# Kernel tuning notes

Measured on AMD Instinct MI355X. Metric: run time of the kernel, lower is better.

## Reference

```python
import jax, jax.numpy as jnp
import numpy as np

K, D = 16384, 128

def setup_inputs() -> dict:
    key = jax.random.key(0)
    k1, k2 = jax.random.split(key)
    parts = jax.random.normal(k1, (K, D), dtype=jnp.float32)
    centers = jax.random.normal(k2, (K, D), dtype=jnp.float32)
    return {"parts": parts, "centers": centers}

def reference(parts, centers):
    # logits[e, j] = parts[e] . centers[j]  -> [K, K]
    logits = jnp.einsum('ed,kd->ek', parts, centers)
    # loss = -mean_e log_softmax(logits[e])[e]  (stable equivalent of
    # log(exp(logits[e,e]) / sum_j exp(logits[e,j])))
    logp = jax.nn.log_softmax(logits, axis=-1)
    diag = jnp.diagonal(logp)  # [K]
    return -jnp.mean(diag)
```

## Files before the change

### kernel.cpp

```cpp
#include <hip/hip_runtime.h>
#include <hip/hip_bf16.h>


#define K_DIM 16384
#define D_DIM 128
#define NSPLIT 32
#define COLS_PER_SPLIT (K_DIM / NSPLIT)
#define TILES_PER_SPLIT (COLS_PER_SPLIT / 32)
#define NROUND (TILES_PER_SPLIT / 2)

typedef __attribute__((ext_vector_type(8)))  int    i32x8;
typedef __attribute__((ext_vector_type(16))) float  f32x16;
typedef __attribute__((ext_vector_type(4)))  float  f32x4;
typedef __attribute__((ext_vector_type(2)))  float  f32x2;

__device__ __forceinline__ unsigned pack_fp8x4(float f0, float f1, float f2, float f3) {
    int r = 0;
    r = __builtin_amdgcn_cvt_pk_fp8_f32(f0, f1, r, false);
    r = __builtin_amdgcn_cvt_pk_fp8_f32(f2, f3, r, true);
    return (unsigned)r;
}

__global__ void convert_kernel(const float* __restrict__ parts,
                               const float* __restrict__ centers,
                               unsigned* __restrict__ pb8,
                               unsigned* __restrict__ cb8,
                               float* __restrict__ rowdot) {
    const float LOG2E = 1.4426950408889634f;
    int i = blockIdx.x * blockDim.x + threadIdx.x;
    const int lane = threadIdx.x & 63;

    f32x4 p = reinterpret_cast<const f32x4*>(parts)[i];
    f32x4 c = reinterpret_cast<const f32x4*>(centers)[i];
    pb8[i] = pack_fp8x4(p[0] * LOG2E, p[1] * LOG2E, p[2] * LOG2E, p[3] * LOG2E);
    cb8[i] = pack_fp8x4(c[0], c[1], c[2], c[3]);

    const int j = (i * 4) >> 7;
    float dd = p[0] * c[0] + p[1] * c[1] + p[2] * c[2] + p[3] * c[3];
#pragma unroll
    for (int off = 16; off > 0; off >>= 1)
        dd += __shfl_xor(dd, off);
    if ((lane & 31) == 0)
        rowdot[j] = dd;
}

__launch_bounds__(256, 4)
__global__ void lse_gemm_kernel(const unsigned char* __restrict__ P8,
                                const unsigned char* __restrict__ C8,
                                float* __restrict__ Sout) {
    __shared__ __attribute__((aligned(128))) unsigned char As[2][2][4096];

    const int bid   = blockIdx.x;
    const int xcd    = bid & 7;
    const int k      = bid >> 3;
    const int split  = xcd * 4 + (k & 3);
    const int rowblk = k >> 2;
    const int tid   = threadIdx.x;
    const int lane  = tid & 63;
    const int w     = tid >> 6;
    const int l31   = lane & 31;
    const int hi    = lane >> 5;
    const int rowgrp = rowblk * 4 + w;
    const int e0    = rowgrp * 64;
    const int e_lo  = e0 + l31;
    const int e_hi  = e0 + 32 + l31;

    i32x8 bl0, bl1, bh0, bh1;
    {
        const unsigned char* plo = P8 + (size_t)e_lo * D_DIM + hi * 32;
        const unsigned char* phi = P8 + (size_t)e_hi * D_DIM + hi * 32;
#pragma unroll
        for (int q = 0; q < 4; ++q) {
            bl0[q]     = reinterpret_cast<const int*>(plo)[q];
            bl1[q]     = reinterpret_cast<const int*>(plo + 64)[q];
            bh0[q]     = reinterpret_cast<const int*>(phi)[q];
            bh1[q]     = reinterpret_cast<const int*>(phi + 64)[q];
            bl0[q + 4] = reinterpret_cast<const int*>(plo + 16)[q];
            bl1[q + 4] = reinterpret_cast<const int*>(plo + 80)[q];
            bh0[q + 4] = reinterpret_cast<const int*>(phi + 16)[q];
            bh1[q + 4] = reinterpret_cast<const int*>(phi + 80)[q];
        }
    }

    const int j0 = split * COLS_PER_SPLIT;
    const int j_w = tid >> 3;
    const int d_w = (tid & 7) * 16;
    const unsigned char* gsrc = C8 + (size_t)(j0 + j_w) * D_DIM + d_w;
    const int woff = j_w * 128 + (d_w ^ ((j_w & 7) << 4));

    const int swz = (l31 & 7) << 4;
    const int rbase = l31 * 128;
    const int rk0a = rbase + (((hi * 32))      ^ swz);
    const int rk0b = rbase + (((hi * 32) + 16) ^ swz);
    const int rk1a = rbase + (((64 + hi * 32))      ^ swz);
    const int rk1b = rbase + (((64 + hi * 32) + 16) ^ swz);

    const f32x16 zc = {};
    float s0 = 0.f, s1 = 0.f;

    auto expsum = [&](const f32x16& acc) -> float {
        f32x2 v0 = {__builtin_amdgcn_exp2f(acc[0]),  __builtin_amdgcn_exp2f(acc[1])};
        f32x2 v1 = {__builtin_amdgcn_exp2f(acc[2]),  __builtin_amdgcn_exp2f(acc[3])};
        f32x2 v2 = {__builtin_amdgcn_exp2f(acc[4]),  __builtin_amdgcn_exp2f(acc[5])};
        f32x2 v3 = {__builtin_amdgcn_exp2f(acc[6]),  __builtin_amdgcn_exp2f(acc[7])};
        f32x2 v4 = {__builtin_amdgcn_exp2f(acc[8]),  __builtin_amdgcn_exp2f(acc[9])};
        f32x2 v5 = {__builtin_amdgcn_exp2f(acc[10]), __builtin_amdgcn_exp2f(acc[11])};
        f32x2 v6 = {__builtin_amdgcn_exp2f(acc[12]), __builtin_amdgcn_exp2f(acc[13])};
        f32x2 v7 = {__builtin_amdgcn_exp2f(acc[14]), __builtin_amdgcn_exp2f(acc[15])};
        v0 += v1; v2 += v3; v4 += v5; v6 += v7;
        v0 += v2; v4 += v6;
        v0 += v4;
        return v0[0] + v0[1];
    };

    auto mfma_tile = [&](const unsigned char* base, f32x16& acc0, f32x16& acc1) {
        i32x8 a0, a1;
#pragma unroll
        for (int q = 0; q < 4; ++q) {
            a0[q]     = reinterpret_cast<const int*>(base + rk0a)[q];
            a0[q + 4] = reinterpret_cast<const int*>(base + rk0b)[q];
            a1[q]     = reinterpret_cast<const int*>(base + rk1a)[q];
            a1[q + 4] = reinterpret_cast<const int*>(base + rk1b)[q];
        }
        acc0 = __builtin_amdgcn_mfma_scale_f32_32x32x64_f8f6f4(
                   a0, bl0, zc,   0, 0, 0, 0x7F, 0, 0x7F);
        acc0 = __builtin_amdgcn_mfma_scale_f32_32x32x64_f8f6f4(
                   a1, bl1, acc0, 0, 0, 0, 0x7F, 0, 0x7F);
        acc1 = __builtin_amdgcn_mfma_scale_f32_32x32x64_f8f6f4(
                   a0, bh0, zc,   0, 0, 0, 0x7F, 0, 0x7F);
        acc1 = __builtin_amdgcn_mfma_scale_f32_32x32x64_f8f6f4(
                   a1, bh1, acc1, 0, 0, 0, 0x7F, 0, 0x7F);
    };

    {
        int4 r0 = *reinterpret_cast<const int4*>(gsrc);
        *reinterpret_cast<int4*>(&As[0][0][woff]) = r0;
        int4 r1 = *reinterpret_cast<const int4*>(gsrc + 32 * D_DIM);
        *reinterpret_cast<int4*>(&As[0][1][woff]) = r1;
    }
    __syncthreads();

    for (int r = 0; r < NROUND; ++r) {
        const int cur = r & 1;
        const int nxt = cur ^ 1;
        const bool pf = (r + 1 < NROUND);
        f32x16 acc0, acc1;

        {
            int4 rg;
            if (pf) rg = *reinterpret_cast<const int4*>(gsrc + (size_t)(2 * r + 2) * 32 * D_DIM);
            mfma_tile(&As[cur][0][0], acc0, acc1);
            if (pf) *reinterpret_cast<int4*>(&As[nxt][0][woff]) = rg;
        }
        s0 += expsum(acc0);
        s1 += expsum(acc1);

        {
            int4 rg;
            if (pf) rg = *reinterpret_cast<const int4*>(gsrc + (size_t)(2 * r + 3) * 32 * D_DIM);
            mfma_tile(&As[cur][1][0], acc0, acc1);
            if (pf) *reinterpret_cast<int4*>(&As[nxt][1][woff]) = rg;
        }
        s0 += expsum(acc0);
        s1 += expsum(acc1);

        __syncthreads();
    }

    s0 += __shfl_xor(s0, 32);
    s1 += __shfl_xor(s1, 32);

    if (lane < 32) {
        Sout[(size_t)e_lo * NSPLIT + split] = s0;
        Sout[(size_t)e_hi * NSPLIT + split] = s1;
    }
}

__global__ void finalize_kernel(const float* __restrict__ Sp,
                                const float* __restrict__ rowdot,
                                float* __restrict__ partial) {
    __shared__ float sm[256];
    const int row = blockIdx.x * 256 + threadIdx.x;

    const f32x4* sp = reinterpret_cast<const f32x4*>(Sp + (size_t)row * NSPLIT);
    float S = 0.0f;
#pragma unroll
    for (int q = 0; q < NSPLIT / 4; ++q) {
        f32x4 v = sp[q];
        S += (v[0] + v[1]) + (v[2] + v[3]);
    }
    const float LN2 = 0.6931471805599453f;
    float loss = LN2 * __builtin_amdgcn_logf(S) - rowdot[row];

    sm[threadIdx.x] = loss;
    __syncthreads();
    for (int off = 128; off > 0; off >>= 1) {
        if (threadIdx.x < off) sm[threadIdx.x] += sm[threadIdx.x + off];
        __syncthreads();
    }
    if (threadIdx.x == 0)
        partial[blockIdx.x] = sm[0];
}

__global__ void reduce_kernel(const float* __restrict__ partial, float* __restrict__ out) {
    const int lane = threadIdx.x;
    float v = partial[lane];
#pragma unroll
    for (int off = 32; off > 0; off >>= 1)
        v += __shfl_xor(v, off);
    if (lane == 0)
        out[0] = v / (float)K_DIM;
}

extern "C" void kernel_launch(void* const* d_in, const int* in_sizes, int n_in,
                              void* d_out, int out_size, void* d_ws, size_t ws_size,
                              hipStream_t stream) {
    const float* parts   = (const float*)d_in[0];
    const float* centers = (const float*)d_in[1];
    float* out = (float*)d_out;

    char* ws = (char*)d_ws;
    unsigned* pb8 = (unsigned*)ws;
    unsigned* cb8 = (unsigned*)(ws + 2u * 1024 * 1024);
    float*  Sp  = (float*)(ws + 4u * 1024 * 1024);
    float*  rowdot  = Sp + (size_t)K_DIM * NSPLIT;
    float*  partial = rowdot + K_DIM;

    const int n4 = (K_DIM * D_DIM) / 4;
    convert_kernel<<<n4 / 256, 256, 0, stream>>>(parts, centers, pb8, cb8, rowdot);
    lse_gemm_kernel<<<(K_DIM / 256) * NSPLIT, 256, 0, stream>>>(
        (const unsigned char*)pb8, (const unsigned char*)cb8, Sp);
    finalize_kernel<<<K_DIM / 256, 256, 0, stream>>>(Sp, rowdot, partial);
    reduce_kernel<<<1, 64, 0, stream>>>(partial, out);
}
```

Measured before the change: 54.69 us.

## Switch to 16x16x128 FP8 MFMA with pre-interleaved centers layout

Replaces the 32x32x64 scaled FP8 MFMA with the 16x16x128 variant, so each wave keeps four 16-row fragments of parts and accumulates four partial exp-sums. The convert kernel now writes centers in an interleaved layout that matches the MFMA operand order. That lets the GEMM copy global memory straight into LDS with linear addressing and no swizzle, and read operands with simple offsets. It also drops the 16-wide accumulators, which should cut register pressure, and interleaves exp2 work with the MFMA issue. The cost is more MFMA instructions and shuffles, and the new LDS read pattern may cause bank conflicts.

```diff
diff --git a/kernel.cpp b/kernel.cpp
--- a/kernel.cpp
+++ b/kernel.cpp
@@ -10,7 +10,6 @@
 #define NROUND (TILES_PER_SPLIT / 2)
 
 typedef __attribute__((ext_vector_type(8)))  int    i32x8;
-typedef __attribute__((ext_vector_type(16))) float  f32x16;
 typedef __attribute__((ext_vector_type(4)))  float  f32x4;
 typedef __attribute__((ext_vector_type(2)))  float  f32x2;
 
@@ -24,7 +23,7 @@
 __global__ void convert_kernel(const float* __restrict__ parts,
                                const float* __restrict__ centers,
                                unsigned* __restrict__ pb8,
-                               unsigned* __restrict__ cb8,
+                               unsigned* __restrict__ cbI8,
                                float* __restrict__ rowdot) {
     const float LOG2E = 1.4426950408889634f;
     int i = blockIdx.x * blockDim.x + threadIdx.x;
@@ -33,9 +32,13 @@
     f32x4 p = reinterpret_cast<const f32x4*>(parts)[i];
     f32x4 c = reinterpret_cast<const f32x4*>(centers)[i];
     pb8[i] = pack_fp8x4(p[0] * LOG2E, p[1] * LOG2E, p[2] * LOG2E, p[3] * LOG2E);
-    cb8[i] = pack_fp8x4(c[0], c[1], c[2], c[3]);
-
-    const int j = (i * 4) >> 7;
+
+    const int e0v = i * 4;
+    const int j   = e0v >> 7;
+    const int d0  = e0v & 127;
+    const int idx = (((j >> 4) * 4 + (d0 >> 5)) * 16 + (j & 15)) * 8 + ((d0 & 31) >> 2);
+    cbI8[idx] = pack_fp8x4(c[0], c[1], c[2], c[3]);
+
     float dd = p[0] * c[0] + p[1] * c[1] + p[2] * c[2] + p[3] * c[3];
 #pragma unroll
     for (int off = 16; off > 0; off >>= 1)
@@ -46,7 +49,7 @@
 
 __launch_bounds__(256, 4)
 __global__ void lse_gemm_kernel(const unsigned char* __restrict__ P8,
-                                const unsigned char* __restrict__ C8,
+                                const unsigned char* __restrict__ CI8,
                                 float* __restrict__ Sout) {
     __shared__ __attribute__((aligned(128))) unsigned char As[2][2][4096];
 
@@ -58,85 +61,69 @@
     const int tid   = threadIdx.x;
     const int lane  = tid & 63;
     const int w     = tid >> 6;
-    const int l31   = lane & 31;
-    const int hi    = lane >> 5;
+    const int l15   = lane & 15;
+    const int lg    = lane >> 4;
     const int rowgrp = rowblk * 4 + w;
     const int e0    = rowgrp * 64;
-    const int e_lo  = e0 + l31;
-    const int e_hi  = e0 + 32 + l31;
-
-    i32x8 bl0, bl1, bh0, bh1;
-    {
-        const unsigned char* plo = P8 + (size_t)e_lo * D_DIM + hi * 32;
-        const unsigned char* phi = P8 + (size_t)e_hi * D_DIM + hi * 32;
+
+    i32x8 bf[4];
+#pragma unroll
+    for (int eb = 0; eb < 4; ++eb) {
+        const unsigned char* pr = P8 + (size_t)(e0 + eb * 16 + l15) * D_DIM + lg * 32;
 #pragma unroll
         for (int q = 0; q < 4; ++q) {
-            bl0[q]     = reinterpret_cast<const int*>(plo)[q];
-            bl1[q]     = reinterpret_cast<const int*>(plo + 64)[q];
-            bh0[q]     = reinterpret_cast<const int*>(phi)[q];
-            bh1[q]     = reinterpret_cast<const int*>(phi + 64)[q];
-            bl0[q + 4] = reinterpret_cast<const int*>(plo + 16)[q];
-            bl1[q + 4] = reinterpret_cast<const int*>(plo + 80)[q];
-            bh0[q + 4] = reinterpret_cast<const int*>(phi + 16)[q];
-            bh1[q + 4] = reinterpret_cast<const int*>(phi + 80)[q];
+            bf[eb][q]     = reinterpret_cast<const int*>(pr)[q];
+            bf[eb][q + 4] = reinterpret_cast<const int*>(pr + 16)[q];
         }
     }
 
     const int j0 = split * COLS_PER_SPLIT;
-    const int j_w = tid >> 3;
-    const int d_w = (tid & 7) * 16;
-    const unsigned char* gsrc = C8 + (size_t)(j0 + j_w) * D_DIM + d_w;
-    const int woff = j_w * 128 + (d_w ^ ((j_w & 7) << 4));
-
-    const int swz = (l31 & 7) << 4;
-    const int rbase = l31 * 128;
-    const int rk0a = rbase + (((hi * 32))      ^ swz);
-    const int rk0b = rbase + (((hi * 32) + 16) ^ swz);
-    const int rk1a = rbase + (((64 + hi * 32))      ^ swz);
-    const int rk1b = rbase + (((64 + hi * 32) + 16) ^ swz);
-
-    const f32x16 zc = {};
-    float s0 = 0.f, s1 = 0.f;
-
-    auto expsum = [&](const f32x16& acc) -> float {
-        f32x2 v0 = {__builtin_amdgcn_exp2f(acc[0]),  __builtin_amdgcn_exp2f(acc[1])};
-        f32x2 v1 = {__builtin_amdgcn_exp2f(acc[2]),  __builtin_amdgcn_exp2f(acc[3])};
-        f32x2 v2 = {__builtin_amdgcn_exp2f(acc[4]),  __builtin_amdgcn_exp2f(acc[5])};
-        f32x2 v3 = {__builtin_amdgcn_exp2f(acc[6]),  __builtin_amdgcn_exp2f(acc[7])};
-        f32x2 v4 = {__builtin_amdgcn_exp2f(acc[8]),  __builtin_amdgcn_exp2f(acc[9])};
-        f32x2 v5 = {__builtin_amdgcn_exp2f(acc[10]), __builtin_amdgcn_exp2f(acc[11])};
-        f32x2 v6 = {__builtin_amdgcn_exp2f(acc[12]), __builtin_amdgcn_exp2f(acc[13])};
-        f32x2 v7 = {__builtin_amdgcn_exp2f(acc[14]), __builtin_amdgcn_exp2f(acc[15])};
-        v0 += v1; v2 += v3; v4 += v5; v6 += v7;
-        v0 += v2; v4 += v6;
-        v0 += v4;
-        return v0[0] + v0[1];
+    const unsigned char* gsrc = CI8 + (size_t)(j0 >> 4) * 2048 + tid * 16;
+    const int ra = l15 * 32 + lg * 512;
+
+    const f32x4 zc = {};
+    float s0 = 0.f, s1 = 0.f, s2 = 0.f, s3 = 0.f;
+
+    auto esum4 = [&](const f32x4& acc) -> float {
+        f32x2 v = {__builtin_amdgcn_exp2f(acc[0]), __builtin_amdgcn_exp2f(acc[1])};
+        f32x2 u = {__builtin_amdgcn_exp2f(acc[2]), __builtin_amdgcn_exp2f(acc[3])};
+        v += u;
+        return v[0] + v[1];
     };
 
-    auto mfma_tile = [&](const unsigned char* base, f32x16& acc0, f32x16& acc1) {
-        i32x8 a0, a1;
+    auto do_tile = [&](const unsigned char* base) {
+        i32x8 aA, aB;
 #pragma unroll
         for (int q = 0; q < 4; ++q) {
-            a0[q]     = reinterpret_cast<const int*>(base + rk0a)[q];
-            a0[q + 4] = reinterpret_cast<const int*>(base + rk0b)[q];
-            a1[q]     = reinterpret_cast<const int*>(base + rk1a)[q];
-            a1[q + 4] = reinterpret_cast<const int*>(base + rk1b)[q];
-        }
-        acc0 = __builtin_amdgcn_mfma_scale_f32_32x32x64_f8f6f4(
-                   a0, bl0, zc,   0, 0, 0, 0x7F, 0, 0x7F);
-        acc0 = __builtin_amdgcn_mfma_scale_f32_32x32x64_f8f6f4(
-                   a1, bl1, acc0, 0, 0, 0, 0x7F, 0, 0x7F);
-        acc1 = __builtin_amdgcn_mfma_scale_f32_32x32x64_f8f6f4(
-                   a0, bh0, zc,   0, 0, 0, 0x7F, 0, 0x7F);
-        acc1 = __builtin_amdgcn_mfma_scale_f32_32x32x64_f8f6f4(
-                   a1, bh1, acc1, 0, 0, 0, 0x7F, 0, 0x7F);
+            aA[q]     = reinterpret_cast<const int*>(base + ra)[q];
+            aA[q + 4] = reinterpret_cast<const int*>(base + ra + 16)[q];
+            aB[q]     = reinterpret_cast<const int*>(base + 2048 + ra)[q];
+            aB[q + 4] = reinterpret_cast<const int*>(base + 2048 + ra + 16)[q];
+        }
+        f32x4 acc;
+        acc = __builtin_amdgcn_mfma_scale_f32_16x16x128_f8f6f4(aA, bf[0], zc, 0, 0, 0, 0x7F, 0, 0x7F);
+        s0 += esum4(acc);
+        acc = __builtin_amdgcn_mfma_scale_f32_16x16x128_f8f6f4(aB, bf[0], zc, 0, 0, 0, 0x7F, 0, 0x7F);
+        s0 += esum4(acc);
+        acc = __builtin_amdgcn_mfma_scale_f32_16x16x128_f8f6f4(aA, bf[1], zc, 0, 0, 0, 0x7F, 0, 0x7F);
+        s1 += esum4(acc);
+        acc = __builtin_amdgcn_mfma_scale_f32_16x16x128_f8f6f4(aB, bf[1], zc, 0, 0, 0, 0x7F, 0, 0x7F);
+        s1 += esum4(acc);
+        acc = __builtin_amdgcn_mfma_scale_f32_16x16x128_f8f6f4(aA, bf[2], zc, 0, 0, 0, 0x7F, 0, 0x7F);
+        s2 += esum4(acc);
+        acc = __builtin_amdgcn_mfma_scale_f32_16x16x128_f8f6f4(aB, bf[2], zc, 0, 0, 0, 0x7F, 0, 0x7F);
+        s2 += esum4(acc);
+        acc = __builtin_amdgcn_mfma_scale_f32_16x16x128_f8f6f4(aA, bf[3], zc, 0, 0, 0, 0x7F, 0, 0x7F);
+        s3 += esum4(acc);
+        acc = __builtin_amdgcn_mfma_scale_f32_16x16x128_f8f6f4(aB, bf[3], zc, 0, 0, 0, 0x7F, 0, 0x7F);
+        s3 += esum4(acc);
     };
 
     {
         int4 r0 = *reinterpret_cast<const int4*>(gsrc);
-        *reinterpret_cast<int4*>(&As[0][0][woff]) = r0;
-        int4 r1 = *reinterpret_cast<const int4*>(gsrc + 32 * D_DIM);
-        *reinterpret_cast<int4*>(&As[0][1][woff]) = r1;
+        *reinterpret_cast<int4*>(&As[0][0][tid * 16]) = r0;
+        int4 r1 = *reinterpret_cast<const int4*>(gsrc + 4096);
+        *reinterpret_cast<int4*>(&As[0][1][tid * 16]) = r1;
     }
     __syncthreads();
 
@@ -144,35 +131,32 @@
         const int cur = r & 1;
         const int nxt = cur ^ 1;
         const bool pf = (r + 1 < NROUND);
-        f32x16 acc0, acc1;
 
         {
             int4 rg;
-            if (pf) rg = *reinterpret_cast<const int4*>(gsrc + (size_t)(2 * r + 2) * 32 * D_DIM);
-            mfma_tile(&As[cur][0][0], acc0, acc1);
-            if (pf) *reinterpret_cast<int4*>(&As[nxt][0][woff]) = rg;
-        }
-        s0 += expsum(acc0);
-        s1 += expsum(acc1);
-
+            if (pf) rg = *reinterpret_cast<const int4*>(gsrc + (size_t)(2 * r + 2) * 4096);
+            do_tile(&As[cur][0][0]);
+            if (pf) *reinterpret_cast<int4*>(&As[nxt][0][tid * 16]) = rg;
+        }
         {
             int4 rg;
-            if (pf) rg = *reinterpret_cast<const int4*>(gsrc + (size_t)(2 * r + 3) * 32 * D_DIM);
-            mfma_tile(&As[cur][1][0], acc0, acc1);
-            if (pf) *reinterpret_cast<int4*>(&As[nxt][1][woff]) = rg;
-        }
-        s0 += expsum(acc0);
-        s1 += expsum(acc1);
-
+            if (pf) rg = *reinterpret_cast<const int4*>(gsrc + (size_t)(2 * r + 3) * 4096);
+            do_tile(&As[cur][1][0]);
+            if (pf) *reinterpret_cast<int4*>(&As[nxt][1][tid * 16]) = rg;
+        }
         __syncthreads();
     }
 
-    s0 += __shfl_xor(s0, 32);
-    s1 += __shfl_xor(s1, 32);
-
-    if (lane < 32) {
-        Sout[(size_t)e_lo * NSPLIT + split] = s0;
-        Sout[(size_t)e_hi * NSPLIT + split] = s1;
+    s0 += __shfl_xor(s0, 16); s0 += __shfl_xor(s0, 32);
+    s1 += __shfl_xor(s1, 16); s1 += __shfl_xor(s1, 32);
+    s2 += __shfl_xor(s2, 16); s2 += __shfl_xor(s2, 32);
+    s3 += __shfl_xor(s3, 16); s3 += __shfl_xor(s3, 32);
+
+    if (lane < 16) {
+        Sout[(size_t)(e0 + lane) * NSPLIT + split]      = s0;
+        Sout[(size_t)(e0 + 16 + lane) * NSPLIT + split] = s1;
+        Sout[(size_t)(e0 + 32 + lane) * NSPLIT + split] = s2;
+        Sout[(size_t)(e0 + 48 + lane) * NSPLIT + split] = s3;
     }
 }
 
@@ -220,16 +204,16 @@
     float* out = (float*)d_out;
 
     char* ws = (char*)d_ws;
-    unsigned* pb8 = (unsigned*)ws;
-    unsigned* cb8 = (unsigned*)(ws + 2u * 1024 * 1024);
+    unsigned* pb8  = (unsigned*)ws;
+    unsigned* cbI8 = (unsigned*)(ws + 2u * 1024 * 1024);
     float*  Sp  = (float*)(ws + 4u * 1024 * 1024);
     float*  rowdot  = Sp + (size_t)K_DIM * NSPLIT;
     float*  partial = rowdot + K_DIM;
 
     const int n4 = (K_DIM * D_DIM) / 4;
-    convert_kernel<<<n4 / 256, 256, 0, stream>>>(parts, centers, pb8, cb8, rowdot);
+    convert_kernel<<<n4 / 256, 256, 0, stream>>>(parts, centers, pb8, cbI8, rowdot);
     lse_gemm_kernel<<<(K_DIM / 256) * NSPLIT, 256, 0, stream>>>(
-        (const unsigned char*)pb8, (const unsigned char*)cb8, Sp);
+        (const unsigned char*)pb8, (const unsigned char*)cbI8, Sp);
     finalize_kernel<<<K_DIM / 256, 256, 0, stream>>>(Sp, rowdot, partial);
     reduce_kernel<<<1, 64, 0, stream>>>(partial, out);
 }
```

Result: no change. 55.39 us (+1.3%).
